# Optimization experiments

Measured on AMD Instinct MI355X. Metric: run time of the kernel, lower is better.

Reference implementation:

```python
import jax, jax.numpy as jnp
import numpy as np
from jax import lax

UP = 4          # upscale_factor (pixel_shuffle factor hardcoded to 4 in ReconBlock)
OUT_CH = UP * UP * 5 * 5  # 400
MID_CH = UP * 5           # 20


def setup_inputs() -> dict:
    key = jax.random.key(0)
    ks = jax.random.split(key, 5)
    B, A, H, W = 2, 5, 96, 96
    pic = jax.random.uniform(ks[0], (B, A, A, H, W), dtype=jnp.float32)
    w1 = jax.random.normal(ks[1], (OUT_CH, 1, 5, 5, 9, 9), dtype=jnp.float32) * 0.02
    b1 = jnp.zeros((OUT_CH,), jnp.float32)
    w2a = jax.random.normal(ks[2], (MID_CH, 1, 3, 3, 5, 5), dtype=jnp.float32) * 0.02
    b2a = jnp.zeros((MID_CH,), jnp.float32)
    w2b = jax.random.normal(ks[3], (OUT_CH, MID_CH, 3, 3, 5, 5), dtype=jnp.float32) * 0.02
    b2b = jnp.zeros((OUT_CH,), jnp.float32)
    return {"pic": pic, "w1": w1, "b1": b1, "w2a": w2a, "b2a": b2a,
            "w2b": w2b, "b2b": b2b}


def _conv4d(x, w):
    # x: [B, Cin, A1, A2, H, W], w: [Cout, Cin, k1, k2, k3, k4], VALID, stride 1
    return lax.conv_general_dilated(x, w, window_strides=(1, 1, 1, 1),
                                    padding='VALID')


def _bias(b):
    return b[None, :, None, None, None, None]


def reference(pic, w1, b1, w2a, b2a, w2b, b2b):
    B, A1, A2, H, W = pic.shape
    # Padder: pad H,W by 4 each side with value 0.5
    padded = jnp.full((B, A1, A2, H + 8, W + 8), 0.5, dtype=pic.dtype)
    padded = padded.at[:, :, :, 4:-4, 4:-4].set(pic)
    x = padded[:, None]  # [B,1,A1,A2,H+8,W+8]

    # DimBlock_1: single 4D conv (5,5,9,9); ReLU defined but never applied
    p1 = _conv4d(x, w1) + _bias(b1)              # [B,400,1,1,H,W]

    # DimBlock_2: two 4D convs (3,3,5,5) with ReLU
    buf = jax.nn.relu(_conv4d(x, w2a) + _bias(b2a))   # [B,20,3,3,H+4,W+4]
    p2 = jax.nn.relu(_conv4d(buf, w2b) + _bias(b2b))  # [B,400,1,1,H,W]

    # BottleNeck
    mid = (p1 + p2) / 2                           # [B,400,1,1,H,W]

    # ReconBlock: take angular position (0,0), pixel_shuffle(4), split 25 -> 5x5
    y = mid[:, :, 0, 0]                           # [B,400,H,W]
    Bc, C, Hh, Ww = y.shape
    r = 4
    y = y.reshape(Bc, 25, r, r, Hh, Ww)
    y = y.transpose(0, 1, 4, 2, 5, 3).reshape(Bc, 25, Hh * r, Ww * r)
    return y.reshape(Bc, 5, 5, Hh * r, Ww * r)
```

## Files before the change

kernel.cpp:

```cpp
#include <hip/hip_runtime.h>
#include <hip/hip_bf16.h>


typedef __attribute__((ext_vector_type(8))) unsigned short ushort8;
typedef __attribute__((ext_vector_type(8))) __bf16 bf16x8;
typedef __attribute__((ext_vector_type(4))) float f32x4;

#define NB 2
#define HSLOT 576
#define HBUF (4 * HSLOT * 8)
#define WST 14336

static __device__ __forceinline__ unsigned short f2bf(float f) {
    __hip_bfloat16 h = __float2bfloat16(f);
    return *reinterpret_cast<unsigned short*>(&h);
}
static __device__ __forceinline__ void gload16(const unsigned short* g, unsigned short* l) {
    __builtin_amdgcn_global_load_lds(
        (const __attribute__((address_space(1))) unsigned int*)(const void*)g,
        (__attribute__((address_space(3))) unsigned int*)(void*)l, 16, 0, 0);
}

__global__ __launch_bounds__(256) void prep_fused_kernel(
    const float* __restrict__ pic, const float* __restrict__ w1,
    const float* __restrict__ w2a, const float* __restrict__ w2b,
    unsigned short* __restrict__ Pn, unsigned short* __restrict__ Wp,
    unsigned short* __restrict__ Wc2) {
    __shared__ unsigned short sT[28544];
    const int blk = blockIdx.x;
    const int tid = threadIdx.x;

    if (blk < 85) {
        int idx = blk * 256 + tid;
        if (idx >= NB * 104 * 104) return;
        int x = idx % 104;
        int y = (idx / 104) % 104;
        int b = idx / (104 * 104);
        unsigned short vals[32];
        bool inter = (y >= 4 && y < 100 && x >= 4 && x < 100);
#pragma unroll
        for (int c = 0; c < 25; ++c) {
            float v = inter ? pic[((b * 25 + c) * 96 + (y - 4)) * 96 + (x - 4)] : 0.5f;
            vals[c] = f2bf(v);
        }
#pragma unroll
        for (int c = 25; c < 32; ++c) vals[c] = 0;
        ushort8* dst = (ushort8*)(Pn + idx * 32);
#pragma unroll
        for (int j = 0; j < 4; ++j) dst[j] = *(ushort8*)&vals[j * 8];
    } else if (blk < 127) {
        int b2 = blk - 85;
        int ocB = b2 % 7, cc = b2 / 7;
        for (int n32 = 0; n32 < 2; ++n32) {
            for (int j = 0; j < 4; ++j) {
                int p  = tid * 4 + j;
                int gl = p >> 5, ol = p & 31;
                int oc = ocB * 64 + n32 * 32 + ol;
                int gp = cc * 32 + gl;
                const float* src = nullptr;
                if (oc < 400 && gp < 180) {
                    int mc = gp % 20, uv = gp / 20;
                    src = w2b + oc * 4500 + (mc * 9 + uv) * 25;
                }
#pragma unroll
                for (int tap = 0; tap < 25; ++tap)
                    sT[(gl * 25 + tap) * 33 + ol] = src ? f2bf(src[tap]) : (unsigned short)0;
            }
            __syncthreads();
            for (int i = 0; i < 13; ++i) {
                int sid = i * 256 + tid;
                if (sid < 3200) {
                    int tap = sid >> 7;
                    int r   = sid & 127;
                    int nb = r >> 6, lane = r & 63;
                    int kq = lane >> 4;
                    int olw = nb * 16 + (lane & 15);
                    unsigned short v8[8];
#pragma unroll
                    for (int e = 0; e < 8; ++e)
                        v8[e] = sT[((kq * 8 + e) * 25 + tap) * 33 + olw];
                    size_t d = (size_t)(cc * 25 + tap) * WST + ocB * 2048 +
                               (n32 * 2 + nb) * 512 + lane * 8;
                    *(ushort8*)(Wp + d) = *(ushort8*)v8;
                }
            }
            __syncthreads();
        }
    } else if (blk < 148) {
        int b3 = blk - 127;
        int ocB = b3 % 7, tt = b3 / 7;
        for (int n32 = 0; n32 < 2; ++n32) {
            for (int j = 0; j < 4; ++j) {
                int p  = tid * 4 + j;
                int cl = p >> 5, ol = p & 31;
                int oc = ocB * 64 + n32 * 32 + ol;
                const float* src = (oc < 400 && cl < 25)
                                       ? (w1 + oc * 2025 + cl * 81 + tt * 27) : nullptr;
#pragma unroll
                for (int tl = 0; tl < 27; ++tl)
                    sT[(cl * 27 + tl) * 33 + ol] = src ? f2bf(src[tl]) : (unsigned short)0;
            }
            __syncthreads();
            for (int i = 0; i < 14; ++i) {
                int sid = i * 256 + tid;
                if (sid < 3456) {
                    int tl = sid >> 7;
                    int r  = sid & 127;
                    int nb = r >> 6, lane = r & 63;
                    int kq = lane >> 4;
                    int olw = nb * 16 + (lane & 15);
                    unsigned short v8[8];
#pragma unroll
                    for (int e = 0; e < 8; ++e)
                        v8[e] = sT[((kq * 8 + e) * 27 + tl) * 33 + olw];
                    int tap_lin = tt * 27 + tl;
                    int dy = tap_lin / 9, dx = tap_lin % 9;
                    int tp = (dx < 5) ? (dy * 5 + dx) : (45 + dy * 4 + (dx - 5));
                    size_t d = (size_t)(150 + tp) * WST + ocB * 2048 +
                               (n32 * 2 + nb) * 512 + lane * 8;
                    *(ushort8*)(Wp + d) = *(ushort8*)v8;
                }
            }
            __syncthreads();
        }
    } else if (blk < 154) {
        int ocB2 = blk - 148;
        if (tid < 128) {
            int lane = tid & 63;
            int oc = ocB2 * 32 + (tid >> 6) * 16 + (lane & 15);
            int kb = (lane >> 4) * 8;
            int uv = oc / 20, mc = oc % 20;
            int u = uv / 3, v = uv % 3;
            const float* wb[8];
#pragma unroll
            for (int e = 0; e < 8; ++e) {
                int k  = kb + e;
                int c1 = k / 5, c2 = k % 5;
                int da1 = c1 - u, da2 = c2 - v;
                bool valid = (oc < 180) && ((unsigned)da1 < 3u) && ((unsigned)da2 < 3u);
                wb[e] = valid ? (w2a + mc * 225 + (da1 * 3 + da2) * 25) : (const float*)0;
            }
            for (int tap = 0; tap < 25; ++tap) {
                unsigned short fr[8];
#pragma unroll
                for (int e = 0; e < 8; ++e) fr[e] = wb[e] ? f2bf(wb[e][tap]) : (unsigned short)0;
                *(ushort8*)(Wc2 + ((size_t)(ocB2 * 25 + tap) * 128 + tid) * 8) = *(ushort8*)fr;
            }
        }
    }
}

__global__ __launch_bounds__(256) void conv2a_mfma_kernel(
    const unsigned short* __restrict__ Pn, const unsigned short* __restrict__ Wc2,
    const float* __restrict__ b2a, unsigned short* __restrict__ Bn) {
    __shared__ __align__(16) unsigned short sHalo[4 * 448 * 8];

    const int tid  = threadIdx.x;
    const int lane = tid & 63, w = tid >> 6;
    const int l15  = lane & 15, lhi = lane >> 4;
    const int gx0  = blockIdx.x;
    const int b    = gx0 / 52, t52 = gx0 % 52;
    const int ty0  = (t52 >> 2) * 8;
    const int tx0  = (t52 & 3) * 32;
    const int ocB  = blockIdx.y;

    for (int L2 = 0; L2 < 7; ++L2) {
        int p = L2 * 64 + lane;
        if (p >= 432) p = 0;
        int hy = (p * 58255) >> 21, hx = p - hy * 36;
        int gy = ty0 + hy; gy = gy > 103 ? 103 : gy;
        int gx = tx0 + hx; gx = gx > 103 ? 103 : gx;
        gload16(Pn + ((size_t)((b * 104 + gy) * 104 + gx)) * 32 + w * 8,
                &sHalo[(w * 448 + L2 * 64) * 8]);
    }
    float bs[2];
#pragma unroll
    for (int n = 0; n < 2; ++n) {
        int oc = ocB * 32 + n * 16 + l15;
        bs[n] = (oc < 180) ? b2a[oc % 20] : 0.f;
    }
    __syncthreads();

    const unsigned short* hb = &sHalo[(lhi * 448 + w * 72 + l15) * 8];
    const unsigned short* wq = Wc2 + (size_t)ocB * 25600 + lane * 8;

    f32x4 acc[4][2] = {};
#pragma unroll
    for (int t = 0; t < 25; ++t) {
        const int u = ((t / 5) * 36 + (t % 5)) * 8;
        bf16x8 a0 = *(const bf16x8*)(hb + u);
        bf16x8 a1 = *(const bf16x8*)(hb + u + 128);
        bf16x8 a2 = *(const bf16x8*)(hb + u + 288);
        bf16x8 a3 = *(const bf16x8*)(hb + u + 416);
        bf16x8 c0 = *(const bf16x8*)(wq);
        bf16x8 c1 = *(const bf16x8*)(wq + 512);
        __builtin_amdgcn_s_setprio(1);
        acc[0][0] = __builtin_amdgcn_mfma_f32_16x16x32_bf16(a0, c0, acc[0][0], 0, 0, 0);
        acc[0][1] = __builtin_amdgcn_mfma_f32_16x16x32_bf16(a0, c1, acc[0][1], 0, 0, 0);
        acc[1][0] = __builtin_amdgcn_mfma_f32_16x16x32_bf16(a1, c0, acc[1][0], 0, 0, 0);
        acc[1][1] = __builtin_amdgcn_mfma_f32_16x16x32_bf16(a1, c1, acc[1][1], 0, 0, 0);
        acc[2][0] = __builtin_amdgcn_mfma_f32_16x16x32_bf16(a2, c0, acc[2][0], 0, 0, 0);
        acc[2][1] = __builtin_amdgcn_mfma_f32_16x16x32_bf16(a2, c1, acc[2][1], 0, 0, 0);
        acc[3][0] = __builtin_amdgcn_mfma_f32_16x16x32_bf16(a3, c0, acc[3][0], 0, 0, 0);
        acc[3][1] = __builtin_amdgcn_mfma_f32_16x16x32_bf16(a3, c1, acc[3][1], 0, 0, 0);
        __builtin_amdgcn_s_setprio(0);
        wq += 1024;
    }

#pragma unroll
    for (int n = 0; n < 2; ++n) {
        int oc = ocB * 32 + n * 16 + l15;
#pragma unroll
        for (int m = 0; m < 4; ++m) {
            int y = ty0 + w * 2 + (m >> 1);
            if (y >= 100) continue;
            int x0 = tx0 + (m & 1) * 16 + lhi * 4;
#pragma unroll
            for (int i = 0; i < 4; ++i) {
                int x = x0 + i;
                if (x >= 100) continue;
                Bn[((size_t)((b * 100 + y) * 100 + x)) * 192 + oc] =
                    f2bf(fmaxf(acc[m][n][i] + bs[n], 0.f));
            }
        }
    }
}

#define MFMA16(A0, A1, A2, A3, B0, B1, B2, B3)                                          \
    {                                                                                   \
        __builtin_amdgcn_s_setprio(1);                                                  \
        acc[0][0] = __builtin_amdgcn_mfma_f32_16x16x32_bf16(A0, B0, acc[0][0], 0, 0, 0);\
        acc[0][1] = __builtin_amdgcn_mfma_f32_16x16x32_bf16(A0, B1, acc[0][1], 0, 0, 0);\
        acc[0][2] = __builtin_amdgcn_mfma_f32_16x16x32_bf16(A0, B2, acc[0][2], 0, 0, 0);\
        acc[0][3] = __builtin_amdgcn_mfma_f32_16x16x32_bf16(A0, B3, acc[0][3], 0, 0, 0);\
        acc[1][0] = __builtin_amdgcn_mfma_f32_16x16x32_bf16(A1, B0, acc[1][0], 0, 0, 0);\
        acc[1][1] = __builtin_amdgcn_mfma_f32_16x16x32_bf16(A1, B1, acc[1][1], 0, 0, 0);\
        acc[1][2] = __builtin_amdgcn_mfma_f32_16x16x32_bf16(A1, B2, acc[1][2], 0, 0, 0);\
        acc[1][3] = __builtin_amdgcn_mfma_f32_16x16x32_bf16(A1, B3, acc[1][3], 0, 0, 0);\
        acc[2][0] = __builtin_amdgcn_mfma_f32_16x16x32_bf16(A2, B0, acc[2][0], 0, 0, 0);\
        acc[2][1] = __builtin_amdgcn_mfma_f32_16x16x32_bf16(A2, B1, acc[2][1], 0, 0, 0);\
        acc[2][2] = __builtin_amdgcn_mfma_f32_16x16x32_bf16(A2, B2, acc[2][2], 0, 0, 0);\
        acc[2][3] = __builtin_amdgcn_mfma_f32_16x16x32_bf16(A2, B3, acc[2][3], 0, 0, 0);\
        acc[3][0] = __builtin_amdgcn_mfma_f32_16x16x32_bf16(A3, B0, acc[3][0], 0, 0, 0);\
        acc[3][1] = __builtin_amdgcn_mfma_f32_16x16x32_bf16(A3, B1, acc[3][1], 0, 0, 0);\
        acc[3][2] = __builtin_amdgcn_mfma_f32_16x16x32_bf16(A3, B2, acc[3][2], 0, 0, 0);\
        acc[3][3] = __builtin_amdgcn_mfma_f32_16x16x32_bf16(A3, B3, acc[3][3], 0, 0, 0);\
        __builtin_amdgcn_s_setprio(0);                                                  \
    }

#define WTAP(HOFF)                                                    \
    {                                                                 \
        wq += WST;                                                    \
        bf16x8 d0 = *(const bf16x8*)(wq);                             \
        bf16x8 d1 = *(const bf16x8*)(wq + 512);                       \
        bf16x8 d2 = *(const bf16x8*)(wq + 1024);                      \
        bf16x8 d3 = *(const bf16x8*)(wq + 1536);                      \
        bf16x8 a0 = *(const bf16x8*)(hb + (HOFF));                    \
        bf16x8 a1 = *(const bf16x8*)(hb + (HOFF) + 128);              \
        bf16x8 a2 = *(const bf16x8*)(hb + (HOFF) + 288);              \
        bf16x8 a3 = *(const bf16x8*)(hb + (HOFF) + 416);              \
        MFMA16(a0, a1, a2, a3, c0, c1, c2, c3);                       \
        c0 = n0; c1 = n1; c2 = n2; c3 = n3;                           \
        n0 = d0; n1 = d1; n2 = d2; n3 = d3;                           \
    }

__global__ __launch_bounds__(256, 2) void conv_mfma_kernel(
    const unsigned short* __restrict__ Pn, const unsigned short* __restrict__ Bn,
    const unsigned short* __restrict__ Wp, const float* __restrict__ b1,
    const float* __restrict__ b2b, float* __restrict__ out) {
    __shared__ __align__(16) unsigned short sHalo[2 * HBUF];

    const int tid  = threadIdx.x;
    const int lane = tid & 63, w = tid >> 6;
    const int l15  = lane & 15, lhi = lane >> 4;
    const int ocB  = blockIdx.y;
    const int pb   = blockIdx.x;
    const int b    = pb / 36;
    const int t36  = pb % 36;
    const int ty0  = (t36 / 3) * 8;
    const int tx0  = (t36 % 3) * 32;

    const int vA = (lhi * HSLOT + w * 72 + l15) * 8;

    auto stageA = [&](int cc, int par) {
        unsigned short* dst0 = &sHalo[par * HBUF + w * HSLOT * 8];
        for (int L2 = 0; L2 < 7; ++L2) {
            int p = L2 * 64 + lane;
            if (p >= 432) p = 0;
            int hy = (p * 58255) >> 21, hx = p - hy * 36;
            gload16(Bn + ((size_t)((b * 100 + ty0 + hy) * 100 + tx0 + hx)) * 192 +
                        cc * 32 + w * 8,
                    dst0 + L2 * 512);
        }
    };
    auto stageB = [&](int seg, int par) {
        int cx = tx0 + (seg == 7 ? 5 : 0);
        unsigned short* dst0 = &sHalo[par * HBUF + w * HSLOT * 8];
        for (int L2 = 0; L2 < 9; ++L2) {
            int p = L2 * 64 + lane;
            int hy = (p * 58255) >> 21, hx = p - hy * 36;
            int gx = cx + hx;
            gx = gx > 103 ? 103 : gx;
            gload16(Pn + ((size_t)((b * 104 + ty0 + hy) * 104 + gx)) * 32 + w * 8,
                    dst0 + L2 * 512);
        }
    };

    float bb2[4], bb1[4];
#pragma unroll
    for (int n = 0; n < 4; ++n) {
        int oc  = ocB * 64 + n * 16 + l15;
        int occ = oc < 400 ? oc : 399;
        bb2[n] = b2b[occ];
        bb1[n] = b1[occ];
    }

    const unsigned short* wq = Wp + ocB * 2048 + lane * 8;
    bf16x8 c0 = *(const bf16x8*)(wq);
    bf16x8 c1 = *(const bf16x8*)(wq + 512);
    bf16x8 c2 = *(const bf16x8*)(wq + 1024);
    bf16x8 c3 = *(const bf16x8*)(wq + 1536);
    bf16x8 n0 = *(const bf16x8*)(wq + WST);
    bf16x8 n1 = *(const bf16x8*)(wq + WST + 512);
    bf16x8 n2 = *(const bf16x8*)(wq + WST + 1024);
    bf16x8 n3 = *(const bf16x8*)(wq + WST + 1536);
    wq += WST;
    stageA(0, 0);
    __syncthreads();

    f32x4 acc[4][4] = {};

    for (int cc = 0; cc < 6; ++cc) {
        const unsigned short* hb = &sHalo[(cc & 1) * HBUF + vA];
        if (cc < 5) stageA(cc + 1, (cc + 1) & 1);
        else        stageB(6, 0);
#pragma unroll
        for (int t = 0; t < 25; ++t)
            WTAP(((t / 5) * 36 + (t % 5)) * 8);
        if (cc == 5) {
#pragma unroll
            for (int m = 0; m < 4; ++m)
#pragma unroll
                for (int n = 0; n < 4; ++n)
#pragma unroll
                    for (int i = 0; i < 4; ++i)
                        acc[m][n][i] = fmaxf(acc[m][n][i] + bb2[n], 0.f);
        }
        asm volatile("s_waitcnt vmcnt(8)" ::: "memory");
        asm volatile("s_barrier" ::: "memory");
    }

    {
        const unsigned short* hb = &sHalo[vA];
        stageB(7, 1);
#pragma unroll
        for (int t = 0; t < 45; ++t)
            WTAP(((t / 5) * 36 + (t % 5)) * 8);
        asm volatile("s_waitcnt vmcnt(8)" ::: "memory");
        asm volatile("s_barrier" ::: "memory");
    }

    {
        const unsigned short* hb = &sHalo[HBUF + vA];
#pragma unroll
        for (int t = 0; t < 36; ++t)
            WTAP(((t >> 2) * 36 + (t & 3)) * 8);
    }

#pragma unroll
    for (int n = 0; n < 4; ++n) {
        int oc = ocB * 64 + n * 16 + l15;
        if (oc >= 400) continue;
        float bv = bb1[n];
        int c25 = oc >> 4, r1 = (oc >> 2) & 3, r2 = oc & 3;
#pragma unroll
        for (int m = 0; m < 4; ++m) {
            int y  = ty0 + w * 2 + (m >> 1);
            int x0 = tx0 + (m & 1) * 16 + lhi * 4;
#pragma unroll
            for (int i = 0; i < 4; ++i) {
                out[((size_t)(b * 25 + c25) * 384 + y * 4 + r1) * 384 + (x0 + i) * 4 + r2] =
                    (acc[m][n][i] + bv) * 0.5f;
            }
        }
    }
}

extern "C" void kernel_launch(void* const* d_in, const int* in_sizes, int n_in,
                              void* d_out, int out_size, void* d_ws, size_t ws_size,
                              hipStream_t stream) {
    const float* pic = (const float*)d_in[0];
    const float* w1  = (const float*)d_in[1];
    const float* b1  = (const float*)d_in[2];
    const float* w2a = (const float*)d_in[3];
    const float* b2a = (const float*)d_in[4];
    const float* w2b = (const float*)d_in[5];
    const float* b2b = (const float*)d_in[6];
    float* out = (float*)d_out;

    char* ws = (char*)d_ws;
    unsigned short* Pn  = (unsigned short*)(ws);
    unsigned short* Bn  = (unsigned short*)(ws + 1384448);
    unsigned short* Wp  = (unsigned short*)(ws + 9064448);
    unsigned short* Wc2 = (unsigned short*)(ws + 15745024);

    prep_fused_kernel<<<154, 256, 0, stream>>>(pic, w1, w2a, w2b, Pn, Wp, Wc2);
    conv2a_mfma_kernel<<<dim3(104, 6), 256, 0, stream>>>(Pn, Wc2, b2a, Bn);
    conv_mfma_kernel<<<dim3(72, 7), 256, 0, stream>>>(Pn, Bn, Wp, b1, b2b, out);
}
```

Measured before the change: 149.4 us.

## Switch conv main loop to 32x32x16 bf16 MFMA with repacked weights

Replaces the 16 per-tap 16x16x32 MFMAs with 8 per-tap 32x32x16 MFMAs. The prep kernel now packs weights in the 32-wide output-channel, 16-k layout those instructions expect, and the halo reads and output scatter are remapped to match. It also drops the one-tap-ahead weight register prefetch (n0..n3) and lowers the vmcnt wait to 4. The aim is fewer LDS A-fragment reads per tap and higher MFMA throughput per instruction. Without the extra prefetch stage, global weight-load latency is less hidden, and the reordered accumulation could expose correctness bugs.

```diff
diff --git a/kernel.cpp b/kernel.cpp
--- a/kernel.cpp
+++ b/kernel.cpp
@@ -5,11 +5,13 @@
 typedef __attribute__((ext_vector_type(8))) unsigned short ushort8;
 typedef __attribute__((ext_vector_type(8))) __bf16 bf16x8;
 typedef __attribute__((ext_vector_type(4))) float f32x4;
+typedef __attribute__((ext_vector_type(16))) float f32x16;
 
 #define NB 2
 #define HSLOT 576
 #define HBUF (4 * HSLOT * 8)
 #define WST 14336
+#define QOFF (2 * HSLOT * 8)
 
 static __device__ __forceinline__ unsigned short f2bf(float f) {
     __hip_bfloat16 h = __float2bfloat16(f);
@@ -72,15 +74,14 @@
                 if (sid < 3200) {
                     int tap = sid >> 7;
                     int r   = sid & 127;
-                    int nb = r >> 6, lane = r & 63;
-                    int kq = lane >> 4;
-                    int olw = nb * 16 + (lane & 15);
+                    int q = r >> 6, lane = r & 63;
+                    int h = lane >> 5, ol = lane & 31;
                     unsigned short v8[8];
 #pragma unroll
                     for (int e = 0; e < 8; ++e)
-                        v8[e] = sT[((kq * 8 + e) * 25 + tap) * 33 + olw];
+                        v8[e] = sT[((q * 16 + h * 8 + e) * 25 + tap) * 33 + ol];
                     size_t d = (size_t)(cc * 25 + tap) * WST + ocB * 2048 +
-                               (n32 * 2 + nb) * 512 + lane * 8;
+                               (q * 2 + n32) * 512 + lane * 8;
                     *(ushort8*)(Wp + d) = *(ushort8*)v8;
                 }
             }
@@ -106,18 +107,19 @@
                 if (sid < 3456) {
                     int tl = sid >> 7;
                     int r  = sid & 127;
-                    int nb = r >> 6, lane = r & 63;
-                    int kq = lane >> 4;
-                    int olw = nb * 16 + (lane & 15);
+                    int q = r >> 6, lane = r & 63;
+                    int h = lane >> 5, ol = lane & 31;
                     unsigned short v8[8];
 #pragma unroll
-                    for (int e = 0; e < 8; ++e)
-                        v8[e] = sT[((kq * 8 + e) * 27 + tl) * 33 + olw];
+                    for (int e = 0; e < 8; ++e) {
+                        int k = q * 16 + h * 8 + e;
+                        v8[e] = (k < 25) ? sT[(k * 27 + tl) * 33 + ol] : (unsigned short)0;
+                    }
                     int tap_lin = tt * 27 + tl;
                     int dy = tap_lin / 9, dx = tap_lin % 9;
                     int tp = (dx < 5) ? (dy * 5 + dx) : (45 + dy * 4 + (dx - 5));
                     size_t d = (size_t)(150 + tp) * WST + ocB * 2048 +
-                               (n32 * 2 + nb) * 512 + lane * 8;
+                               (q * 2 + n32) * 512 + lane * 8;
                     *(ushort8*)(Wp + d) = *(ushort8*)v8;
                 }
             }
@@ -226,26 +228,18 @@
     }
 }
 
-#define MFMA16(A0, A1, A2, A3, B0, B1, B2, B3)                                          \
-    {                                                                                   \
-        __builtin_amdgcn_s_setprio(1);                                                  \
-        acc[0][0] = __builtin_amdgcn_mfma_f32_16x16x32_bf16(A0, B0, acc[0][0], 0, 0, 0);\
-        acc[0][1] = __builtin_amdgcn_mfma_f32_16x16x32_bf16(A0, B1, acc[0][1], 0, 0, 0);\
-        acc[0][2] = __builtin_amdgcn_mfma_f32_16x16x32_bf16(A0, B2, acc[0][2], 0, 0, 0);\
-        acc[0][3] = __builtin_amdgcn_mfma_f32_16x16x32_bf16(A0, B3, acc[0][3], 0, 0, 0);\
-        acc[1][0] = __builtin_amdgcn_mfma_f32_16x16x32_bf16(A1, B0, acc[1][0], 0, 0, 0);\
-        acc[1][1] = __builtin_amdgcn_mfma_f32_16x16x32_bf16(A1, B1, acc[1][1], 0, 0, 0);\
-        acc[1][2] = __builtin_amdgcn_mfma_f32_16x16x32_bf16(A1, B2, acc[1][2], 0, 0, 0);\
-        acc[1][3] = __builtin_amdgcn_mfma_f32_16x16x32_bf16(A1, B3, acc[1][3], 0, 0, 0);\
-        acc[2][0] = __builtin_amdgcn_mfma_f32_16x16x32_bf16(A2, B0, acc[2][0], 0, 0, 0);\
-        acc[2][1] = __builtin_amdgcn_mfma_f32_16x16x32_bf16(A2, B1, acc[2][1], 0, 0, 0);\
-        acc[2][2] = __builtin_amdgcn_mfma_f32_16x16x32_bf16(A2, B2, acc[2][2], 0, 0, 0);\
-        acc[2][3] = __builtin_amdgcn_mfma_f32_16x16x32_bf16(A2, B3, acc[2][3], 0, 0, 0);\
-        acc[3][0] = __builtin_amdgcn_mfma_f32_16x16x32_bf16(A3, B0, acc[3][0], 0, 0, 0);\
-        acc[3][1] = __builtin_amdgcn_mfma_f32_16x16x32_bf16(A3, B1, acc[3][1], 0, 0, 0);\
-        acc[3][2] = __builtin_amdgcn_mfma_f32_16x16x32_bf16(A3, B2, acc[3][2], 0, 0, 0);\
-        acc[3][3] = __builtin_amdgcn_mfma_f32_16x16x32_bf16(A3, B3, acc[3][3], 0, 0, 0);\
-        __builtin_amdgcn_s_setprio(0);                                                  \
+#define MFMA8()                                                                          \
+    {                                                                                    \
+        __builtin_amdgcn_s_setprio(1);                                                   \
+        acc[0][0] = __builtin_amdgcn_mfma_f32_32x32x16_bf16(a00, c0, acc[0][0], 0, 0, 0);\
+        acc[0][1] = __builtin_amdgcn_mfma_f32_32x32x16_bf16(a00, c1, acc[0][1], 0, 0, 0);\
+        acc[1][0] = __builtin_amdgcn_mfma_f32_32x32x16_bf16(a01, c0, acc[1][0], 0, 0, 0);\
+        acc[1][1] = __builtin_amdgcn_mfma_f32_32x32x16_bf16(a01, c1, acc[1][1], 0, 0, 0);\
+        acc[0][0] = __builtin_amdgcn_mfma_f32_32x32x16_bf16(a10, c2, acc[0][0], 0, 0, 0);\
+        acc[0][1] = __builtin_amdgcn_mfma_f32_32x32x16_bf16(a10, c3, acc[0][1], 0, 0, 0);\
+        acc[1][0] = __builtin_amdgcn_mfma_f32_32x32x16_bf16(a11, c2, acc[1][0], 0, 0, 0);\
+        acc[1][1] = __builtin_amdgcn_mfma_f32_32x32x16_bf16(a11, c3, acc[1][1], 0, 0, 0);\
+        __builtin_amdgcn_s_setprio(0);                                                   \
     }
 
 #define WTAP(HOFF)                                                    \
@@ -255,13 +249,12 @@
         bf16x8 d1 = *(const bf16x8*)(wq + 512);                       \
         bf16x8 d2 = *(const bf16x8*)(wq + 1024);                      \
         bf16x8 d3 = *(const bf16x8*)(wq + 1536);                      \
-        bf16x8 a0 = *(const bf16x8*)(hb + (HOFF));                    \
-        bf16x8 a1 = *(const bf16x8*)(hb + (HOFF) + 128);              \
-        bf16x8 a2 = *(const bf16x8*)(hb + (HOFF) + 288);              \
-        bf16x8 a3 = *(const bf16x8*)(hb + (HOFF) + 416);              \
-        MFMA16(a0, a1, a2, a3, c0, c1, c2, c3);                       \
-        c0 = n0; c1 = n1; c2 = n2; c3 = n3;                           \
-        n0 = d0; n1 = d1; n2 = d2; n3 = d3;                           \
+        bf16x8 a00 = *(const bf16x8*)(hb + (HOFF));                   \
+        bf16x8 a01 = *(const bf16x8*)(hb + (HOFF) + 288);             \
+        bf16x8 a10 = *(const bf16x8*)(hb + (HOFF) + QOFF);            \
+        bf16x8 a11 = *(const bf16x8*)(hb + (HOFF) + QOFF + 288);      \
+        MFMA8();                                                      \
+        c0 = d0; c1 = d1; c2 = d2; c3 = d3;                           \
     }
 
 __global__ __launch_bounds__(256, 2) void conv_mfma_kernel(
@@ -272,7 +265,7 @@
 
     const int tid  = threadIdx.x;
     const int lane = tid & 63, w = tid >> 6;
-    const int l15  = lane & 15, lhi = lane >> 4;
+    const int l31  = lane & 31, h = lane >> 5;
     const int ocB  = blockIdx.y;
     const int pb   = blockIdx.x;
     const int b    = pb / 36;
@@ -280,7 +273,7 @@
     const int ty0  = (t36 / 3) * 8;
     const int tx0  = (t36 % 3) * 32;
 
-    const int vA = (lhi * HSLOT + w * 72 + l15) * 8;
+    const int vA = (h * HSLOT + w * 72 + l31) * 8;
 
     auto stageA = [&](int cc, int par) {
         unsigned short* dst0 = &sHalo[par * HBUF + w * HSLOT * 8];
@@ -306,10 +299,10 @@
         }
     };
 
-    float bb2[4], bb1[4];
-#pragma unroll
-    for (int n = 0; n < 4; ++n) {
-        int oc  = ocB * 64 + n * 16 + l15;
+    float bb2[2], bb1[2];
+#pragma unroll
+    for (int n = 0; n < 2; ++n) {
+        int oc  = ocB * 64 + n * 32 + l31;
         int occ = oc < 400 ? oc : 399;
         bb2[n] = b2b[occ];
         bb1[n] = b1[occ];
@@ -320,15 +313,10 @@
     bf16x8 c1 = *(const bf16x8*)(wq + 512);
     bf16x8 c2 = *(const bf16x8*)(wq + 1024);
     bf16x8 c3 = *(const bf16x8*)(wq + 1536);
-    bf16x8 n0 = *(const bf16x8*)(wq + WST);
-    bf16x8 n1 = *(const bf16x8*)(wq + WST + 512);
-    bf16x8 n2 = *(const bf16x8*)(wq + WST + 1024);
-    bf16x8 n3 = *(const bf16x8*)(wq + WST + 1536);
-    wq += WST;
     stageA(0, 0);
     __syncthreads();
 
-    f32x4 acc[4][4] = {};
+    f32x16 acc[2][2] = {};
 
     for (int cc = 0; cc < 6; ++cc) {
         const unsigned short* hb = &sHalo[(cc & 1) * HBUF + vA];
@@ -339,14 +327,14 @@
             WTAP(((t / 5) * 36 + (t % 5)) * 8);
         if (cc == 5) {
 #pragma unroll
-            for (int m = 0; m < 4; ++m)
-#pragma unroll
-                for (int n = 0; n < 4; ++n)
-#pragma unroll
-                    for (int i = 0; i < 4; ++i)
+            for (int m = 0; m < 2; ++m)
+#pragma unroll
+                for (int n = 0; n < 2; ++n)
+#pragma unroll
+                    for (int i = 0; i < 16; ++i)
                         acc[m][n][i] = fmaxf(acc[m][n][i] + bb2[n], 0.f);
         }
-        asm volatile("s_waitcnt vmcnt(8)" ::: "memory");
+        asm volatile("s_waitcnt vmcnt(4)" ::: "memory");
         asm volatile("s_barrier" ::: "memory");
     }
 
@@ -356,7 +344,7 @@
 #pragma unroll
         for (int t = 0; t < 45; ++t)
             WTAP(((t / 5) * 36 + (t % 5)) * 8);
-        asm volatile("s_waitcnt vmcnt(8)" ::: "memory");
+        asm volatile("s_waitcnt vmcnt(4)" ::: "memory");
         asm volatile("s_barrier" ::: "memory");
     }
 
@@ -368,19 +356,19 @@
     }
 
 #pragma unroll
-    for (int n = 0; n < 4; ++n) {
-        int oc = ocB * 64 + n * 16 + l15;
+    for (int n = 0; n < 2; ++n) {
+        int oc = ocB * 64 + n * 32 + l31;
         if (oc >= 400) continue;
         float bv = bb1[n];
         int c25 = oc >> 4, r1 = (oc >> 2) & 3, r2 = oc & 3;
 #pragma unroll
-        for (int m = 0; m < 4; ++m) {
-            int y  = ty0 + w * 2 + (m >> 1);
-            int x0 = tx0 + (m & 1) * 16 + lhi * 4;
-#pragma unroll
-            for (int i = 0; i < 4; ++i) {
-                out[((size_t)(b * 25 + c25) * 384 + y * 4 + r1) * 384 + (x0 + i) * 4 + r2] =
-                    (acc[m][n][i] + bv) * 0.5f;
+        for (int m = 0; m < 2; ++m) {
+            int y = ty0 + w * 2 + m;
+#pragma unroll
+            for (int reg = 0; reg < 16; ++reg) {
+                int x = tx0 + (reg & 3) + 8 * (reg >> 2) + 4 * h;
+                out[((size_t)(b * 25 + c25) * 384 + y * 4 + r1) * 384 + x * 4 + r2] =
+                    (acc[m][n][reg] + bv) * 0.5f;
             }
         }
     }
```

New measurement: 165.6 us. 1.11x slower.
